# Kernel optimization log

Measured on AMD Instinct MI355X. Metric: run time of the kernel, lower is better.

Reference implementation:

```python
import jax, jax.numpy as jnp
import numpy as np

N_P, N_A, N_S, D = 50000, 25000, 1, 64
ALPHA = 0.2  # leaky_relu negative slope
E_P2P, E_P2A, E_A2P, E_A2A = 800000, 400000, 400000, 400000


def _gat(z_msg, wh_dst, aw, src, dst, n_dst):
    """Per-edge-type GAT: score = leaky_relu(attn_fc([z_src ; Wh_dst])),
    segment softmax over destination, weighted scatter-sum of z_src.
    Attention linear is split into src/dst halves and applied per-node (cheaper)."""
    d = z_msg.shape[1]
    e = (z_msg @ aw[:d])[src] + (wh_dst @ aw[d:])[dst]  # [E]
    e = jnp.where(e > 0, e, ALPHA * e)                   # leaky_relu
    m = jax.ops.segment_max(e, dst, num_segments=n_dst)
    ex = jnp.exp(e - m[dst])
    den = jax.ops.segment_sum(ex, dst, num_segments=n_dst)
    w = ex / den[dst]                                    # per-dst softmax (mailbox softmax)
    return jax.ops.segment_sum(w[:, None] * z_msg[src], dst, num_segments=n_dst)


def setup_inputs() -> dict:
    ks = jax.random.split(jax.random.key(0), 32)
    sc = 1.0 / np.sqrt(D)
    f32, i32 = jnp.float32, jnp.int32
    inp = {
        "feat_P": jax.random.normal(ks[0], (N_P, D), f32),
        "feat_A": jax.random.normal(ks[1], (N_A, D), f32),
        "feat_state": jax.random.normal(ks[2], (N_S, D), f32),
    }
    for i, n in enumerate(["P", "A", "p2p", "p2a", "a2p", "a2a", "p2s", "a2s", "in"]):
        inp["W_" + n] = jax.random.normal(ks[3 + i], (D, D), f32) * sc
        inp["b_" + n] = jnp.zeros((D,), f32)
    for i, n in enumerate(["p2p", "p2a", "a2p", "a2a", "p2s", "a2s"]):
        inp["a_" + n] = jax.random.normal(ks[12 + i], (2 * D,), f32) * sc
    inp["src_p2p"] = jax.random.randint(ks[18], (E_P2P,), 0, N_P, i32)
    inp["dst_p2p"] = jax.random.randint(ks[19], (E_P2P,), 0, N_P, i32)
    inp["src_p2a"] = jax.random.randint(ks[20], (E_P2A,), 0, N_P, i32)
    inp["dst_p2a"] = jax.random.randint(ks[21], (E_P2A,), 0, N_A, i32)
    inp["src_a2p"] = jax.random.randint(ks[22], (E_A2P,), 0, N_A, i32)
    inp["dst_a2p"] = jax.random.randint(ks[23], (E_A2P,), 0, N_P, i32)
    inp["src_a2a"] = jax.random.randint(ks[24], (E_A2A,), 0, N_A, i32)
    inp["dst_a2a"] = jax.random.randint(ks[25], (E_A2A,), 0, N_A, i32)
    inp["src_p2s"] = jnp.arange(N_P, dtype=i32)
    inp["dst_p2s"] = jnp.zeros((N_P,), i32)
    inp["src_a2s"] = jnp.arange(N_A, dtype=i32)
    inp["dst_a2s"] = jnp.zeros((N_A,), i32)
    return inp


def reference(feat_P, feat_A, feat_state,
              W_P, b_P, W_A, b_A, W_p2p, b_p2p, W_p2a, b_p2a, W_a2p, b_a2p,
              W_a2a, b_a2a, W_p2s, b_p2s, W_a2s, b_a2s, W_in, b_in,
              a_p2p, a_p2a, a_a2p, a_a2a, a_p2s, a_a2s,
              src_p2p, dst_p2p, src_p2a, dst_p2a, src_a2p, dst_a2p,
              src_a2a, dst_a2a, src_p2s, dst_p2s, src_a2s, dst_a2s):
    Wh_P = feat_P @ W_P + b_P          # self transform per node type
    Wh_A = feat_A @ W_A + b_A
    Wh_in = feat_state @ W_in + b_in   # 'in' self-loop message to state
    h_P = jax.nn.relu(
        Wh_P
        + _gat(feat_P @ W_p2p + b_p2p, Wh_P, a_p2p, src_p2p, dst_p2p, N_P)
        + _gat(feat_A @ W_a2p + b_a2p, Wh_P, a_a2p, src_a2p, dst_a2p, N_P))
    h_A = jax.nn.relu(
        Wh_A
        + _gat(feat_P @ W_p2a + b_p2a, Wh_A, a_p2a, src_p2a, dst_p2a, N_A)
        + _gat(feat_A @ W_a2a + b_a2a, Wh_A, a_a2a, src_a2a, dst_a2a, N_A))
    h_S = jax.nn.relu(
        Wh_in
        + _gat(feat_P @ W_p2s + b_p2s, Wh_in, a_p2s, src_p2s, dst_p2s, N_S)
        + _gat(feat_A @ W_a2s + b_a2s, Wh_in, a_a2s, src_a2s, dst_a2s, N_S))
    return (h_P, h_A, h_S)
```

## Files before the change

### kernel.cpp

```cpp
#include <hip/hip_runtime.h>
#include <math.h>

#define ALPHA 0.2f
#define NP 50000
#define NA 25000
#define NBINS 150000
#define ABASE 100000
#define NBUCK 586
#define CH 4096
#define CAP 8192
#define GP ((NP + 63) / 64)
#define GA ((NA + 63) / 64)
#define XS_LD 68

typedef unsigned short u16;
typedef __attribute__((ext_vector_type(8))) short bf16x8;
typedef __attribute__((ext_vector_type(8))) unsigned short u16x8;
typedef __attribute__((ext_vector_type(4))) float f32x4;

__device__ __forceinline__ float bf2f(u16 u) { return __uint_as_float(((unsigned)u) << 16); }
__device__ __forceinline__ u16 f2bf(float f) {
    unsigned x = __float_as_uint(f);
    return (u16)((x + 0x7fffu + ((x >> 16) & 1u)) >> 16);
}

struct FrontArgs {
    const float *feat_P, *feat_A, *feat_S;
    const float *W_P, *b_P, *W_A, *b_A, *W_p2p, *b_p2p, *W_p2a, *b_p2a,
                *W_a2p, *b_a2p, *W_a2a, *b_a2a, *W_p2s, *b_p2s, *W_a2s, *b_a2s,
                *W_in, *b_in;
    const float *a_p2p, *a_p2a, *a_a2p, *a_a2a, *a_p2s, *a_a2s;
    float *WhP, *WhA;
    u16 *z_p2p, *z_p2a, *z_a2p, *z_a2a;
    float *ss_p2p, *sd_p2p, *ss_p2a, *sd_p2a, *ss_a2p, *sd_a2p, *ss_a2a, *sd_a2a;
    float *outS, *den2, *numP, *numA;
    const int *src_p2p, *dst_p2p, *src_a2p, *dst_a2p,
              *src_p2a, *dst_p2a, *src_a2a, *dst_a2a;
    int E_p2p, E_a2p, E_p2a, E_a2a, E_tot, nblk;
    int *cursor0, *ebuf;
};

__device__ __forceinline__ void xform_body(int bid, float* __restrict__ Xs,
    const float* __restrict__ X, int N,
    const float* __restrict__ W0, const float* __restrict__ b0, float* __restrict__ Wh,
    const float* __restrict__ dA, float* __restrict__ sdA,
    const float* __restrict__ dB, float* __restrict__ sdB,
    const float* __restrict__ W1, const float* __restrict__ b1, u16* __restrict__ z1,
    const float* __restrict__ v1, float* __restrict__ s1,
    const float* __restrict__ W2, const float* __restrict__ b2, u16* __restrict__ z2,
    const float* __restrict__ v2, float* __restrict__ s2,
    const float* __restrict__ W3, const float* __restrict__ b3,
    const float* __restrict__ v3,
    const float* __restrict__ aD,
    const float* __restrict__ fS, const float* __restrict__ W_in, const float* __restrict__ b_in,
    float* __restrict__ num, float* __restrict__ den)
{
    int tid = threadIdx.x, wv = tid >> 6, lane = tid & 63;
    int g = lane >> 4, li = lane & 15;
    const float* Wm = wv == 0 ? W0 : wv == 1 ? W1 : wv == 2 ? W2 : W3;
    const float* bm = wv == 0 ? b0 : wv == 1 ? b1 : wv == 2 ? b2 : b3;
    const float* dv = wv == 0 ? dA : wv == 1 ? v1 : wv == 2 ? v2 : v3;
    float* sm       = wv == 0 ? sdA : wv == 1 ? s1 : wv == 2 ? s2 : nullptr;
    u16* zm         = wv == 1 ? z1 : wv == 2 ? z2 : nullptr;

    int base0 = bid * 64;
    for (int i = tid; i < 4096; i += 256) {
        int r = i >> 6, c = i & 63;
        int rowC = min(base0 + r, N - 1);
        Xs[r * XS_LD + c] = X[(long long)rowC * 64 + c];
    }

    bf16x8 Bf[4][2];
#pragma unroll
    for (int cb = 0; cb < 4; ++cb)
#pragma unroll
        for (int kc = 0; kc < 2; ++kc) {
            bf16x8 t;
#pragma unroll
            for (int j = 0; j < 8; ++j)
                t[j] = (short)f2bf(Wm[(kc * 32 + g * 8 + j) * 64 + cb * 16 + li]);
            Bf[cb][kc] = t;
        }
    float bl[4], dvl[4], dbl[4];
#pragma unroll
    for (int cb = 0; cb < 4; ++cb) {
        bl[cb]  = bm[cb * 16 + li];
        dvl[cb] = dv[cb * 16 + li];
        dbl[cb] = (wv == 0) ? dB[cb * 16 + li] : 0.f;
    }
    float sdst = 0.f;
    if (wv == 3) {
#pragma unroll
        for (int cb = 0; cb < 4; ++cb) {
            int c = cb * 16 + li;
            float a = b_in[c];
            for (int k = 0; k < 64; ++k) a = fmaf(fS[k], W_in[k * 64 + c], a);
            sdst = fmaf(a, aD[c], sdst);
        }
#pragma unroll
        for (int o = 1; o < 16; o <<= 1) sdst += __shfl_xor(sdst, o, 64);
    }
    float pnum[4] = {0.f, 0.f, 0.f, 0.f};
    float pden = 0.f;
    __syncthreads();

#pragma unroll
    for (int rt = 0; rt < 4; ++rt) {
        int rbase = base0 + rt * 16;
        if (rbase >= N) break;
        bf16x8 Af[2];
#pragma unroll
        for (int kc = 0; kc < 2; ++kc) {
            const float* xp = &Xs[(rt * 16 + li) * XS_LD + kc * 32 + g * 8];
            bf16x8 t;
#pragma unroll
            for (int j = 0; j < 8; ++j)
                t[j] = (short)f2bf(xp[j]);
            Af[kc] = t;
        }
        f32x4 acc[4] = {{0,0,0,0},{0,0,0,0},{0,0,0,0},{0,0,0,0}};
#pragma unroll
        for (int kc = 0; kc < 2; ++kc)
#pragma unroll
            for (int cb = 0; cb < 4; ++cb)
                acc[cb] = __builtin_amdgcn_mfma_f32_16x16x32_bf16(Af[kc], Bf[cb][kc], acc[cb], 0, 0, 0);
        float pd[4] = {0,0,0,0}, pb[4] = {0,0,0,0};
#pragma unroll
        for (int cb = 0; cb < 4; ++cb)
#pragma unroll
            for (int r = 0; r < 4; ++r) {
                float val = acc[cb][r] + bl[cb];
                acc[cb][r] = val;
                pd[r] = fmaf(val, dvl[cb], pd[r]);
                pb[r] = fmaf(val, dbl[cb], pb[r]);
            }
#pragma unroll
        for (int o = 1; o < 16; o <<= 1)
#pragma unroll
            for (int r = 0; r < 4; ++r) {
                pd[r] += __shfl_xor(pd[r], o, 64);
                pb[r] += __shfl_xor(pb[r], o, 64);
            }
        int rg = rbase + g * 4;
        if (wv == 3) {
#pragma unroll
            for (int r = 0; r < 4; ++r) {
                int row = rg + r;
                float e = pd[r] + sdst;
                e = e > 0.f ? e : ALPHA * e;
                float w = (row < N) ? __expf(e) : 0.f;
                pden += w;
#pragma unroll
                for (int cb = 0; cb < 4; ++cb)
                    pnum[cb] = fmaf(w, acc[cb][r], pnum[cb]);
            }
            continue;
        }
        if (li == 0) {
#pragma unroll
            for (int r = 0; r < 4; ++r) {
                int row = rg + r;
                if (row < N) {
                    sm[row] = pd[r];
                    if (wv == 0) sdB[row] = pb[r];
                }
            }
        }
        if (wv == 0) {
#pragma unroll
            for (int r = 0; r < 4; ++r) {
                int row = rg + r;
                if (row < N)
#pragma unroll
                    for (int cb = 0; cb < 4; ++cb)
                        Wh[(long long)row * 64 + cb * 16 + li] = acc[cb][r];
            }
        } else {
#pragma unroll
            for (int r = 0; r < 4; ++r) {
                int row = rg + r;
                if (row < N)
#pragma unroll
                    for (int cb = 0; cb < 4; ++cb)
                        zm[(long long)row * 64 + cb * 16 + li] = f2bf(acc[cb][r]);
            }
        }
    }
    if (wv == 3) {
#pragma unroll
        for (int o = 16; o <= 32; o <<= 1) {
            pden += __shfl_xor(pden, o, 64);
#pragma unroll
            for (int cb = 0; cb < 4; ++cb)
                pnum[cb] += __shfl_xor(pnum[cb], o, 64);
        }
        if (lane < 16) {
#pragma unroll
            for (int cb = 0; cb < 4; ++cb)
                atomicAdd(&num[cb * 16 + li], pnum[cb]);
            if (li == 0) atomicAdd(den, pden);
        }
    }
}

__device__ __forceinline__ void edge_decode(int k,
    const int* __restrict__ s0, const int* __restrict__ d0, int E0,
    const int* __restrict__ s1, const int* __restrict__ d1, int E1,
    const int* __restrict__ s2, const int* __restrict__ d2, int E2,
    const int* __restrict__ s3, const int* __restrict__ d3,
    int& src, int& bin) {
    if (k < E0) { src = s0[k]; bin = 2 * d0[k]; return; }
    k -= E0; if (k < E1) { src = s1[k]; bin = 2 * d1[k] + 1; return; }
    k -= E1; if (k < E2) { src = s2[k]; bin = ABASE + 2 * d2[k]; return; }
    k -= E2; src = s3[k]; bin = ABASE + 2 * d3[k] + 1;
}

__global__ __launch_bounds__(256) void fused_front(FrontArgs A) {
    __shared__ float smem[64 * XS_LD];
    int bid = blockIdx.x;
    int tid = threadIdx.x;
    if (bid < A.nblk) {
        int* h = (int*)smem;
        int* base = h + NBUCK;
        for (int i = tid; i < NBUCK; i += 256) h[i] = 0;
        __syncthreads();
        int b0 = bid * CH;
        int b1 = min(b0 + CH, A.E_tot);
        int cbin[16], csrc[16];
#pragma unroll
        for (int it = 0; it < 16; ++it) {
            int i = b0 + it * 256 + tid;
            int bin = -1, src = 0;
            if (i < b1)
                edge_decode(i, A.src_p2p, A.dst_p2p, A.E_p2p,
                            A.src_a2p, A.dst_a2p, A.E_a2p,
                            A.src_p2a, A.dst_p2a, A.E_p2a,
                            A.src_a2a, A.dst_a2a, src, bin);
            cbin[it] = bin; csrc[it] = src;
            if (bin >= 0) atomicAdd(&h[bin >> 8], 1);
        }
        __syncthreads();
        for (int i = tid; i < NBUCK; i += 256) {
            int c = h[i];
            base[i] = c ? (i * CAP + atomicAdd(&A.cursor0[i], c)) : 0;
            h[i] = 0;
        }
        __syncthreads();
#pragma unroll
        for (int it = 0; it < 16; ++it) {
            int bin = cbin[it];
            if (bin >= 0) {
                int bk = bin >> 8;
                int pos = base[bk] + atomicAdd(&h[bk], 1);
                if (pos < (bk + 1) * CAP)
                    A.ebuf[pos] = csrc[it] | ((bin & 255) << 16);
            }
        }
        return;
    }
    bid -= A.nblk;
    if (bid < GP) {
        xform_body(bid, smem, A.feat_P, NP,
                   A.W_P, A.b_P, A.WhP, A.a_p2p + 64, A.sd_p2p, A.a_a2p + 64, A.sd_a2p,
                   A.W_p2p, A.b_p2p, A.z_p2p, A.a_p2p, A.ss_p2p,
                   A.W_p2a, A.b_p2a, A.z_p2a, A.a_p2a, A.ss_p2a,
                   A.W_p2s, A.b_p2s, A.a_p2s, A.a_p2s + 64,
                   A.feat_S, A.W_in, A.b_in, A.numP, &A.den2[0]);
        return;
    }
    bid -= GP;
    if (bid < GA) {
        xform_body(bid, smem, A.feat_A, NA,
                   A.W_A, A.b_A, A.WhA, A.a_p2a + 64, A.sd_p2a, A.a_a2a + 64, A.sd_a2a,
                   A.W_a2p, A.b_a2p, A.z_a2p, A.a_a2p, A.ss_a2p,
                   A.W_a2a, A.b_a2a, A.z_a2a, A.a_a2a, A.ss_a2a,
                   A.W_a2s, A.b_a2s, A.a_a2s, A.a_a2s + 64,
                   A.feat_S, A.W_in, A.b_in, A.numA, &A.den2[1]);
        return;
    }
    if (tid < 64) {
        int c = tid;
        float acc = A.b_in[c];
        for (int k = 0; k < 64; ++k) acc = fmaf(A.feat_S[k], A.W_in[k * 64 + c], acc);
        A.outS[c] = acc;
    }
}

__device__ void scan_counts(const int* __restrict__ counts, int* sstart) {
    __shared__ int wtot_sb[4];
    int tid = threadIdx.x, lane = tid & 63, wv = tid >> 6;
    int carry = 0;
    for (int c = 0; c < 3; ++c) {
        int i = c * 256 + tid;
        int v = (i < NBUCK) ? min(counts[i], CAP) : 0;
        int x = v;
#pragma unroll
        for (int o = 1; o < 64; o <<= 1) {
            int y = __shfl_up(x, o, 64);
            if (lane >= o) x += y;
        }
        if (lane == 63) wtot_sb[wv] = x;
        __syncthreads();
        int woff = carry;
        for (int j = 0; j < wv; ++j) woff += wtot_sb[j];
        int ctot = wtot_sb[0] + wtot_sb[1] + wtot_sb[2] + wtot_sb[3];
        if (i < NBUCK) sstart[i] = x + woff - v;
        __syncthreads();
        carry += ctot;
    }
    if (tid == 0) sstart[NBUCK] = carry;
    __syncthreads();
}

__global__ __launch_bounds__(256) void fused_mid(
    const int* __restrict__ ebuf, const int* __restrict__ cursor0,
    int* __restrict__ ssrc, int* __restrict__ offs,
    const float* __restrict__ numP, const float* __restrict__ numA,
    const float* __restrict__ den2, float* __restrict__ outS) {
    int tid = threadIdx.x, lane = tid & 63, wv = tid >> 6;
    if ((int)blockIdx.x >= NBUCK) {
        if (tid < 64)
            outS[tid] = fmaxf(outS[tid] + numP[tid] / den2[0] + numA[tid] / den2[1], 0.f);
        return;
    }
    __shared__ int sstart[NBUCK + 1];
    __shared__ int lsrc[CAP];
    __shared__ int lcnt[256];
    __shared__ int loff[256];
    __shared__ int lcur[256];
    __shared__ int wtot[4];
    int b = blockIdx.x;
    scan_counts(cursor0, sstart);
    int pstart = sstart[b];
    int rstart = b * CAP;
    int cnt = min(cursor0[b], CAP);
    lcnt[tid] = 0;
    __syncthreads();
    for (int e = tid; e < cnt; e += 256)
        atomicAdd(&lcnt[((unsigned)ebuf[rstart + e]) >> 16], 1);
    __syncthreads();
    int v = lcnt[tid];
    int x = v;
#pragma unroll
    for (int o = 1; o < 64; o <<= 1) {
        int y = __shfl_up(x, o, 64);
        if (lane >= o) x += y;
    }
    if (lane == 63) wtot[wv] = x;
    __syncthreads();
    int woff = 0;
    for (int j = 0; j < wv; ++j) woff += wtot[j];
    int excl = x + woff - v;
    loff[tid] = excl;
    lcur[tid] = excl;
    __syncthreads();
    for (int e = tid; e < cnt; e += 256) {
        int val = ebuf[rstart + e];
        int pos = atomicAdd(&lcur[((unsigned)val) >> 16], 1);
        lsrc[pos] = val & 0xFFFF;
    }
    __syncthreads();
    for (int i = tid; i < cnt; i += 256) ssrc[pstart + i] = lsrc[i];
    int gb = b * 256 + tid;
    if (gb < NBINS) offs[gb] = pstart + loff[tid];
    if (b == 0 && tid == 0) offs[NBINS] = sstart[NBUCK];
}

__device__ __forceinline__ void seg_gat_g8(const int* __restrict__ ssrc, int s0, int s1,
                                           const float* __restrict__ ss, float sd,
                                           const u16* __restrict__ z, int lane,
                                           float* __restrict__ acc) {
    int cnt = s1 - s0;
    if (cnt <= 0) return;
    int egrp = lane >> 3, cg8 = (lane & 7) * 8;
    if (cnt <= 64) {
        int s = 0; float w = 0.f;
        if (lane < cnt) {
            s = ssrc[s0 + lane];
            float e = ss[s] + sd;
            e = e > 0.f ? e : ALPHA * e;
            w = __expf(e);
        }
        float den = w;
#pragma unroll
        for (int o = 32; o > 0; o >>= 1) den += __shfl_xor(den, o, 64);
        w *= 1.f / den;
        int nit = (cnt + 7) >> 3;
        for (int it = 0; it < nit; ++it) {
            int ei = it * 8 + egrp;
            float wt = __shfl(w, ei, 64);
            int   st = __shfl(s, ei, 64);
            u16x8 q = *(const u16x8*)(z + (long long)st * 64 + cg8);
#pragma unroll
            for (int j = 0; j < 8; ++j)
                acc[j] = fmaf(wt, bf2f(q[j]), acc[j]);
        }
    } else {
        float den = 0.f;
        for (int i = s0 + lane; i < s1; i += 64) {
            float e = ss[ssrc[i]] + sd; e = e > 0.f ? e : ALPHA * e; den += __expf(e);
        }
#pragma unroll
        for (int o = 32; o > 0; o >>= 1) den += __shfl_xor(den, o, 64);
        float inv = 1.f / den;
        for (int c = s0; c < s1; c += 64) {
            int i = c + lane; int s = 0; float w = 0.f;
            if (i < s1) {
                s = ssrc[i];
                float e = ss[s] + sd; e = e > 0.f ? e : ALPHA * e;
                w = __expf(e) * inv;
            }
            int cc = min(64, s1 - c);
            int nit = (cc + 7) >> 3;
            for (int it = 0; it < nit; ++it) {
                int ei = it * 8 + egrp;
                float wt = __shfl(w, ei, 64);
                int   st = __shfl(s, ei, 64);
                u16x8 q = *(const u16x8*)(z + (long long)st * 64 + cg8);
#pragma unroll
                for (int j = 0; j < 8; ++j)
                    acc[j] = fmaf(wt, bf2f(q[j]), acc[j]);
            }
        }
    }
}

__global__ __launch_bounds__(256) void gat_all(
    const int* __restrict__ ssrc, const int* __restrict__ offs,
    const float* __restrict__ WhP, float* __restrict__ outP,
    const float* __restrict__ WhA, float* __restrict__ outA,
    const float* __restrict__ ss_p2p, const float* __restrict__ sd_p2p, const u16* __restrict__ z_p2p,
    const float* __restrict__ ss_a2p, const float* __restrict__ sd_a2p, const u16* __restrict__ z_a2p,
    const float* __restrict__ ss_p2a, const float* __restrict__ sd_p2a, const u16* __restrict__ z_p2a,
    const float* __restrict__ ss_a2a, const float* __restrict__ sd_a2a, const u16* __restrict__ z_a2a) {
    int lane = threadIdx.x & 63;
    int g = (blockIdx.x * blockDim.x + threadIdx.x) >> 6;
    if (g >= NP + NA) return;
    bool isP = g < NP;
    int d = isP ? g : g - NP;
    int bin0 = isP ? 2 * d : ABASE + 2 * d;
    int e0 = offs[bin0], e1 = offs[bin0 + 1], e2 = offs[bin0 + 2];
    float acc[8] = {0.f, 0.f, 0.f, 0.f, 0.f, 0.f, 0.f, 0.f};
    if (isP) {
        seg_gat_g8(ssrc, e0, e1, ss_p2p, sd_p2p[d], z_p2p, lane, acc);
        seg_gat_g8(ssrc, e1, e2, ss_a2p, sd_a2p[d], z_a2p, lane, acc);
    } else {
        seg_gat_g8(ssrc, e0, e1, ss_p2a, sd_p2a[d], z_p2a, lane, acc);
        seg_gat_g8(ssrc, e1, e2, ss_a2a, sd_a2a[d], z_a2a, lane, acc);
    }
#pragma unroll
    for (int o = 8; o <= 32; o <<= 1)
#pragma unroll
        for (int j = 0; j < 8; ++j)
            acc[j] += __shfl_xor(acc[j], o, 64);
    if (lane < 8) {
        const float* Wh = isP ? WhP : WhA;
        float* outp = isP ? outP : outA;
        const float* sp = &Wh[(long long)d * 64 + lane * 8];
        float4 s0v = *(const float4*)sp;
        float4 s1v = *(const float4*)(sp + 4);
        float4 r0, r1;
        r0.x = fmaxf(s0v.x + acc[0], 0.f); r0.y = fmaxf(s0v.y + acc[1], 0.f);
        r0.z = fmaxf(s0v.z + acc[2], 0.f); r0.w = fmaxf(s0v.w + acc[3], 0.f);
        r1.x = fmaxf(s1v.x + acc[4], 0.f); r1.y = fmaxf(s1v.y + acc[5], 0.f);
        r1.z = fmaxf(s1v.z + acc[6], 0.f); r1.w = fmaxf(s1v.w + acc[7], 0.f);
        float* op = &outp[(long long)d * 64 + lane * 8];
        *(float4*)op = r0;
        *(float4*)(op + 4) = r1;
    }
}

extern "C" void kernel_launch(void* const* d_in, const int* in_sizes, int n_in,
                              void* d_out, int out_size, void* d_ws, size_t ws_size,
                              hipStream_t stream) {
    const float* feat_P = (const float*)d_in[0];
    const float* feat_A = (const float*)d_in[1];
    const float* feat_S = (const float*)d_in[2];
    const float* W_P   = (const float*)d_in[3];  const float* b_P   = (const float*)d_in[4];
    const float* W_A   = (const float*)d_in[5];  const float* b_A   = (const float*)d_in[6];
    const float* W_p2p = (const float*)d_in[7];  const float* b_p2p = (const float*)d_in[8];
    const float* W_p2a = (const float*)d_in[9];  const float* b_p2a = (const float*)d_in[10];
    const float* W_a2p = (const float*)d_in[11]; const float* b_a2p = (const float*)d_in[12];
    const float* W_a2a = (const float*)d_in[13]; const float* b_a2a = (const float*)d_in[14];
    const float* W_p2s = (const float*)d_in[15]; const float* b_p2s = (const float*)d_in[16];
    const float* W_a2s = (const float*)d_in[17]; const float* b_a2s = (const float*)d_in[18];
    const float* W_in  = (const float*)d_in[19]; const float* b_in  = (const float*)d_in[20];
    const float* a_p2p = (const float*)d_in[21];
    const float* a_p2a = (const float*)d_in[22];
    const float* a_a2p = (const float*)d_in[23];
    const float* a_a2a = (const float*)d_in[24];
    const float* a_p2s = (const float*)d_in[25];
    const float* a_a2s = (const float*)d_in[26];
    const int* src_p2p = (const int*)d_in[27]; const int* dst_p2p = (const int*)d_in[28];
    const int* src_p2a = (const int*)d_in[29]; const int* dst_p2a = (const int*)d_in[30];
    const int* src_a2p = (const int*)d_in[31]; const int* dst_a2p = (const int*)d_in[32];
    const int* src_a2a = (const int*)d_in[33]; const int* dst_a2a = (const int*)d_in[34];
    int E_p2p = in_sizes[27], E_p2a = in_sizes[29], E_a2p = in_sizes[31], E_a2a = in_sizes[33];
    int E_tot = E_p2p + E_a2p + E_p2a + E_a2a;

    float* out = (float*)d_out;
    float* outP = out;
    float* outA = out + (long long)NP * 64;
    float* outS = out + (long long)(NP + NA) * 64;

    float* ws = (float*)d_ws;
    float* WhP = ws; ws += (long long)NP * 64;
    float* WhA = ws; ws += (long long)NA * 64;
    u16* z_p2p = (u16*)ws; ws += (long long)NP * 32;
    u16* z_p2a = (u16*)ws; ws += (long long)NP * 32;
    u16* z_a2p = (u16*)ws; ws += (long long)NA * 32;
    u16* z_a2a = (u16*)ws; ws += (long long)NA * 32;
    float* ss_p2p = ws; ws += NP;  float* sd_p2p = ws; ws += NP;
    float* ss_p2a = ws; ws += NP;  float* sd_p2a = ws; ws += NA;
    float* ss_a2p = ws; ws += NA;  float* sd_a2p = ws; ws += NP;
    float* ss_a2a = ws; ws += NA;  float* sd_a2a = ws; ws += NA;
    float* zreg = ws;
    int*   cursor0 = (int*)ws; ws += NBUCK;
    float* den2 = ws; ws += 2;
    float* numP = ws; ws += 64;
    float* numA = ws; ws += 64;
    size_t zbytes = (size_t)((char*)ws - (char*)zreg);
    int* iw = (int*)ws;
    int* ebuf = iw; iw += NBUCK * CAP;
    int* ssrc = iw; iw += E_tot;
    int* offs = iw; iw += NBINS + 1;

    const int T = 256;
    int nblk = (E_tot + CH - 1) / CH;

    hipMemsetAsync(zreg, 0, zbytes, stream);

    FrontArgs FA;
    FA.feat_P = feat_P; FA.feat_A = feat_A; FA.feat_S = feat_S;
    FA.W_P = W_P; FA.b_P = b_P; FA.W_A = W_A; FA.b_A = b_A;
    FA.W_p2p = W_p2p; FA.b_p2p = b_p2p; FA.W_p2a = W_p2a; FA.b_p2a = b_p2a;
    FA.W_a2p = W_a2p; FA.b_a2p = b_a2p; FA.W_a2a = W_a2a; FA.b_a2a = b_a2a;
    FA.W_p2s = W_p2s; FA.b_p2s = b_p2s; FA.W_a2s = W_a2s; FA.b_a2s = b_a2s;
    FA.W_in = W_in; FA.b_in = b_in;
    FA.a_p2p = a_p2p; FA.a_p2a = a_p2a; FA.a_a2p = a_a2p; FA.a_a2a = a_a2a;
    FA.a_p2s = a_p2s; FA.a_a2s = a_a2s;
    FA.WhP = WhP; FA.WhA = WhA;
    FA.z_p2p = z_p2p; FA.z_p2a = z_p2a;
    FA.z_a2p = z_a2p; FA.z_a2a = z_a2a;
    FA.ss_p2p = ss_p2p; FA.sd_p2p = sd_p2p; FA.ss_p2a = ss_p2a; FA.sd_p2a = sd_p2a;
    FA.ss_a2p = ss_a2p; FA.sd_a2p = sd_a2p; FA.ss_a2a = ss_a2a; FA.sd_a2a = sd_a2a;
    FA.outS = outS; FA.den2 = den2; FA.numP = numP; FA.numA = numA;
    FA.src_p2p = src_p2p; FA.dst_p2p = dst_p2p; FA.src_a2p = src_a2p; FA.dst_a2p = dst_a2p;
    FA.src_p2a = src_p2a; FA.dst_p2a = dst_p2a; FA.src_a2a = src_a2a; FA.dst_a2a = dst_a2a;
    FA.E_p2p = E_p2p; FA.E_a2p = E_a2p; FA.E_p2a = E_p2a; FA.E_a2a = E_a2a;
    FA.E_tot = E_tot; FA.nblk = nblk;
    FA.cursor0 = cursor0; FA.ebuf = ebuf;
    fused_front<<<nblk + GP + GA + 1, T, 0, stream>>>(FA);

    fused_mid<<<NBUCK + 1, T, 0, stream>>>(ebuf, cursor0, ssrc, offs,
                                           numP, numA, den2, outS);

    gat_all<<<((NP + NA) * 64 + T - 1) / T, T, 0, stream>>>(ssrc, offs,
        WhP, outP, WhA, outA,
        ss_p2p, sd_p2p, z_p2p, ss_a2p, sd_a2p, z_a2p,
        ss_p2a, sd_p2a, z_p2a, ss_a2a, sd_a2a, z_a2a);
}
```

Before: 159.7 us.

## Reassociate state-node GAT through raw features and rebalance front/mid kernels

```diff
diff --git a/kernel.cpp b/kernel.cpp
--- a/kernel.cpp
+++ b/kernel.cpp
@@ -11,7 +11,8 @@
 #define CAP 8192
 #define GP ((NP + 63) / 64)
 #define GA ((NA + 63) / 64)
-#define XS_LD 68
+#define SB_P 384
+#define SB_A 192
 
 typedef unsigned short u16;
 typedef __attribute__((ext_vector_type(8))) short bf16x8;
@@ -24,184 +25,29 @@
     return (u16)((x + 0x7fffu + ((x >> 16) & 1u)) >> 16);
 }
 
-struct FrontArgs {
+struct K1Args {
+    const int *s0, *d0, *s1, *d1, *s2, *d2, *s3, *d3;
+    int E0, E1, E2, E3, Etot, nblk;
+    int *cursor0, *ebuf;
+    const float *feat_P, *feat_A, *feat_S;
+    const float *W_p2s, *b_p2s, *a_p2s, *W_a2s, *b_a2s, *a_a2s, *W_in, *b_in;
+    float *numP, *numA, *den2;
+};
+
+struct K2Args {
+    const int *ebuf; const int *cursor0;
+    int *ssrc; int *offs;
     const float *feat_P, *feat_A, *feat_S;
     const float *W_P, *b_P, *W_A, *b_A, *W_p2p, *b_p2p, *W_p2a, *b_p2a,
                 *W_a2p, *b_a2p, *W_a2a, *b_a2a, *W_p2s, *b_p2s, *W_a2s, *b_a2s,
                 *W_in, *b_in;
-    const float *a_p2p, *a_p2a, *a_a2p, *a_a2a, *a_p2s, *a_a2s;
+    const float *a_p2p, *a_p2a, *a_a2p, *a_a2a;
     float *WhP, *WhA;
     u16 *z_p2p, *z_p2a, *z_a2p, *z_a2a;
     float *ss_p2p, *sd_p2p, *ss_p2a, *sd_p2a, *ss_a2p, *sd_a2p, *ss_a2a, *sd_a2a;
-    float *outS, *den2, *numP, *numA;
-    const int *src_p2p, *dst_p2p, *src_a2p, *dst_a2p,
-              *src_p2a, *dst_p2a, *src_a2a, *dst_a2a;
-    int E_p2p, E_a2p, E_p2a, E_a2a, E_tot, nblk;
-    int *cursor0, *ebuf;
+    const float *numP, *numA, *den2;
+    float *outS;
 };
-
-__device__ __forceinline__ void xform_body(int bid, float* __restrict__ Xs,
-    const float* __restrict__ X, int N,
-    const float* __restrict__ W0, const float* __restrict__ b0, float* __restrict__ Wh,
-    const float* __restrict__ dA, float* __restrict__ sdA,
-    const float* __restrict__ dB, float* __restrict__ sdB,
-    const float* __restrict__ W1, const float* __restrict__ b1, u16* __restrict__ z1,
-    const float* __restrict__ v1, float* __restrict__ s1,
-    const float* __restrict__ W2, const float* __restrict__ b2, u16* __restrict__ z2,
-    const float* __restrict__ v2, float* __restrict__ s2,
-    const float* __restrict__ W3, const float* __restrict__ b3,
-    const float* __restrict__ v3,
-    const float* __restrict__ aD,
-    const float* __restrict__ fS, const float* __restrict__ W_in, const float* __restrict__ b_in,
-    float* __restrict__ num, float* __restrict__ den)
-{
-    int tid = threadIdx.x, wv = tid >> 6, lane = tid & 63;
-    int g = lane >> 4, li = lane & 15;
-    const float* Wm = wv == 0 ? W0 : wv == 1 ? W1 : wv == 2 ? W2 : W3;
-    const float* bm = wv == 0 ? b0 : wv == 1 ? b1 : wv == 2 ? b2 : b3;
-    const float* dv = wv == 0 ? dA : wv == 1 ? v1 : wv == 2 ? v2 : v3;
-    float* sm       = wv == 0 ? sdA : wv == 1 ? s1 : wv == 2 ? s2 : nullptr;
-    u16* zm         = wv == 1 ? z1 : wv == 2 ? z2 : nullptr;
-
-    int base0 = bid * 64;
-    for (int i = tid; i < 4096; i += 256) {
-        int r = i >> 6, c = i & 63;
-        int rowC = min(base0 + r, N - 1);
-        Xs[r * XS_LD + c] = X[(long long)rowC * 64 + c];
-    }
-
-    bf16x8 Bf[4][2];
-#pragma unroll
-    for (int cb = 0; cb < 4; ++cb)
-#pragma unroll
-        for (int kc = 0; kc < 2; ++kc) {
-            bf16x8 t;
-#pragma unroll
-            for (int j = 0; j < 8; ++j)
-                t[j] = (short)f2bf(Wm[(kc * 32 + g * 8 + j) * 64 + cb * 16 + li]);
-            Bf[cb][kc] = t;
-        }
-    float bl[4], dvl[4], dbl[4];
-#pragma unroll
-    for (int cb = 0; cb < 4; ++cb) {
-        bl[cb]  = bm[cb * 16 + li];
-        dvl[cb] = dv[cb * 16 + li];
-        dbl[cb] = (wv == 0) ? dB[cb * 16 + li] : 0.f;
-    }
-    float sdst = 0.f;
-    if (wv == 3) {
-#pragma unroll
-        for (int cb = 0; cb < 4; ++cb) {
-            int c = cb * 16 + li;
-            float a = b_in[c];
-            for (int k = 0; k < 64; ++k) a = fmaf(fS[k], W_in[k * 64 + c], a);
-            sdst = fmaf(a, aD[c], sdst);
-        }
-#pragma unroll
-        for (int o = 1; o < 16; o <<= 1) sdst += __shfl_xor(sdst, o, 64);
-    }
-    float pnum[4] = {0.f, 0.f, 0.f, 0.f};
-    float pden = 0.f;
-    __syncthreads();
-
-#pragma unroll
-    for (int rt = 0; rt < 4; ++rt) {
-        int rbase = base0 + rt * 16;
-        if (rbase >= N) break;
-        bf16x8 Af[2];
-#pragma unroll
-        for (int kc = 0; kc < 2; ++kc) {
-            const float* xp = &Xs[(rt * 16 + li) * XS_LD + kc * 32 + g * 8];
-            bf16x8 t;
-#pragma unroll
-            for (int j = 0; j < 8; ++j)
-                t[j] = (short)f2bf(xp[j]);
-            Af[kc] = t;
-        }
-        f32x4 acc[4] = {{0,0,0,0},{0,0,0,0},{0,0,0,0},{0,0,0,0}};
-#pragma unroll
-        for (int kc = 0; kc < 2; ++kc)
-#pragma unroll
-            for (int cb = 0; cb < 4; ++cb)
-                acc[cb] = __builtin_amdgcn_mfma_f32_16x16x32_bf16(Af[kc], Bf[cb][kc], acc[cb], 0, 0, 0);
-        float pd[4] = {0,0,0,0}, pb[4] = {0,0,0,0};
-#pragma unroll
-        for (int cb = 0; cb < 4; ++cb)
-#pragma unroll
-            for (int r = 0; r < 4; ++r) {
-                float val = acc[cb][r] + bl[cb];
-                acc[cb][r] = val;
-                pd[r] = fmaf(val, dvl[cb], pd[r]);
-                pb[r] = fmaf(val, dbl[cb], pb[r]);
-            }
-#pragma unroll
-        for (int o = 1; o < 16; o <<= 1)
-#pragma unroll
-            for (int r = 0; r < 4; ++r) {
-                pd[r] += __shfl_xor(pd[r], o, 64);
-                pb[r] += __shfl_xor(pb[r], o, 64);
-            }
-        int rg = rbase + g * 4;
-        if (wv == 3) {
-#pragma unroll
-            for (int r = 0; r < 4; ++r) {
-                int row = rg + r;
-                float e = pd[r] + sdst;
-                e = e > 0.f ? e : ALPHA * e;
-                float w = (row < N) ? __expf(e) : 0.f;
-                pden += w;
-#pragma unroll
-                for (int cb = 0; cb < 4; ++cb)
-                    pnum[cb] = fmaf(w, acc[cb][r], pnum[cb]);
-            }
-            continue;
-        }
-        if (li == 0) {
-#pragma unroll
-            for (int r = 0; r < 4; ++r) {
-                int row = rg + r;
-                if (row < N) {
-                    sm[row] = pd[r];
-                    if (wv == 0) sdB[row] = pb[r];
-                }
-            }
-        }
-        if (wv == 0) {
-#pragma unroll
-            for (int r = 0; r < 4; ++r) {
-                int row = rg + r;
-                if (row < N)
-#pragma unroll
-                    for (int cb = 0; cb < 4; ++cb)
-                        Wh[(long long)row * 64 + cb * 16 + li] = acc[cb][r];
-            }
-        } else {
-#pragma unroll
-            for (int r = 0; r < 4; ++r) {
-                int row = rg + r;
-                if (row < N)
-#pragma unroll
-                    for (int cb = 0; cb < 4; ++cb)
-                        zm[(long long)row * 64 + cb * 16 + li] = f2bf(acc[cb][r]);
-            }
-        }
-    }
-    if (wv == 3) {
-#pragma unroll
-        for (int o = 16; o <= 32; o <<= 1) {
-            pden += __shfl_xor(pden, o, 64);
-#pragma unroll
-            for (int cb = 0; cb < 4; ++cb)
-                pnum[cb] += __shfl_xor(pnum[cb], o, 64);
-        }
-        if (lane < 16) {
-#pragma unroll
-            for (int cb = 0; cb < 4; ++cb)
-                atomicAdd(&num[cb * 16 + li], pnum[cb]);
-            if (li == 0) atomicAdd(den, pden);
-        }
-    }
-}
 
 __device__ __forceinline__ void edge_decode(int k,
     const int* __restrict__ s0, const int* __restrict__ d0, int E0,
@@ -215,27 +61,24 @@
     k -= E2; src = s3[k]; bin = ABASE + 2 * d3[k] + 1;
 }
 
-__global__ __launch_bounds__(256) void fused_front(FrontArgs A) {
-    __shared__ float smem[64 * XS_LD];
+__global__ __launch_bounds__(256) void k1_kernel(K1Args A) {
+    __shared__ int h[NBUCK];
+    __shared__ int base[NBUCK];
     int bid = blockIdx.x;
     int tid = threadIdx.x;
     if (bid < A.nblk) {
-        int* h = (int*)smem;
-        int* base = h + NBUCK;
         for (int i = tid; i < NBUCK; i += 256) h[i] = 0;
         __syncthreads();
         int b0 = bid * CH;
-        int b1 = min(b0 + CH, A.E_tot);
+        int b1 = min(b0 + CH, A.Etot);
         int cbin[16], csrc[16];
 #pragma unroll
         for (int it = 0; it < 16; ++it) {
             int i = b0 + it * 256 + tid;
             int bin = -1, src = 0;
             if (i < b1)
-                edge_decode(i, A.src_p2p, A.dst_p2p, A.E_p2p,
-                            A.src_a2p, A.dst_a2p, A.E_a2p,
-                            A.src_p2a, A.dst_p2a, A.E_p2a,
-                            A.src_a2a, A.dst_a2a, src, bin);
+                edge_decode(i, A.s0, A.d0, A.E0, A.s1, A.d1, A.E1,
+                            A.s2, A.d2, A.E2, A.s3, A.d3, src, bin);
             cbin[it] = bin; csrc[it] = src;
             if (bin >= 0) atomicAdd(&h[bin >> 8], 1);
         }
@@ -258,32 +101,52 @@
         }
         return;
     }
-    bid -= A.nblk;
-    if (bid < GP) {
-        xform_body(bid, smem, A.feat_P, NP,
-                   A.W_P, A.b_P, A.WhP, A.a_p2p + 64, A.sd_p2p, A.a_a2p + 64, A.sd_a2p,
-                   A.W_p2p, A.b_p2p, A.z_p2p, A.a_p2p, A.ss_p2p,
-                   A.W_p2a, A.b_p2a, A.z_p2a, A.a_p2a, A.ss_p2a,
-                   A.W_p2s, A.b_p2s, A.a_p2s, A.a_p2s + 64,
-                   A.feat_S, A.W_in, A.b_in, A.numP, &A.den2[0]);
-        return;
-    }
-    bid -= GP;
-    if (bid < GA) {
-        xform_body(bid, smem, A.feat_A, NA,
-                   A.W_A, A.b_A, A.WhA, A.a_p2a + 64, A.sd_p2a, A.a_a2a + 64, A.sd_a2a,
-                   A.W_a2p, A.b_a2p, A.z_a2p, A.a_a2p, A.ss_a2p,
-                   A.W_a2a, A.b_a2a, A.z_a2a, A.a_a2a, A.ss_a2a,
-                   A.W_a2s, A.b_a2s, A.a_a2s, A.a_a2s + 64,
-                   A.feat_S, A.W_in, A.b_in, A.numA, &A.den2[1]);
-        return;
-    }
+    float* red = (float*)h;
+    int sb = bid - A.nblk;
+    bool isP = sb < SB_P;
+    int bidl = isP ? sb : sb - SB_P;
+    int nb = isP ? SB_P : SB_A;
+    int N = isP ? NP : NA;
+    const float* X   = isP ? A.feat_P : A.feat_A;
+    const float* W   = isP ? A.W_p2s  : A.W_a2s;
+    const float* b   = isP ? A.b_p2s  : A.b_a2s;
+    const float* a   = isP ? A.a_p2s  : A.a_a2s;
+    float* num       = isP ? A.numP   : A.numA;
+    float* den       = isP ? &A.den2[0] : &A.den2[1];
+    int lane = tid & 63, wv = tid >> 6;
+    float v = 0.f;
+    for (int c = 0; c < 64; ++c) v = fmaf(W[lane * 64 + c], a[c], v);
+    float t0 = b[lane] * a[lane];
+    float whc = A.b_in[lane];
+    for (int k = 0; k < 64; ++k) whc = fmaf(A.feat_S[k], A.W_in[k * 64 + lane], whc);
+    float t1 = whc * a[64 + lane];
+#pragma unroll
+    for (int o = 1; o < 64; o <<= 1) {
+        t0 += __shfl_xor(t0, o, 64);
+        t1 += __shfl_xor(t1, o, 64);
+    }
+    float cbias = t0 + t1;
+    float accx = 0.f, accd = 0.f;
+    int gw = bidl * 4 + wv, waves = nb * 4;
+    for (int r = gw; r < N; r += waves) {
+        float x = X[(long long)r * 64 + lane];
+        float ss = x * v;
+#pragma unroll
+        for (int o = 1; o < 64; o <<= 1) ss += __shfl_xor(ss, o, 64);
+        float e = ss + cbias;
+        e = e > 0.f ? e : ALPHA * e;
+        float w = __expf(e);
+        accx = fmaf(w, x, accx);
+        accd += w;
+    }
+    red[wv * 64 + lane] = accx;
+    if (lane == 0) red[256 + wv] = accd;
+    __syncthreads();
     if (tid < 64) {
-        int c = tid;
-        float acc = A.b_in[c];
-        for (int k = 0; k < 64; ++k) acc = fmaf(A.feat_S[k], A.W_in[k * 64 + c], acc);
-        A.outS[c] = acc;
-    }
+        float t = red[tid] + red[64 + tid] + red[128 + tid] + red[192 + tid];
+        atomicAdd(&num[tid], t);
+    }
+    if (tid == 64) atomicAdd(den, red[256] + red[257] + red[258] + red[259]);
 }
 
 __device__ void scan_counts(const int* __restrict__ counts, int* sstart) {
@@ -312,58 +175,194 @@
     __syncthreads();
 }
 
-__global__ __launch_bounds__(256) void fused_mid(
-    const int* __restrict__ ebuf, const int* __restrict__ cursor0,
-    int* __restrict__ ssrc, int* __restrict__ offs,
-    const float* __restrict__ numP, const float* __restrict__ numA,
-    const float* __restrict__ den2, float* __restrict__ outS) {
+__device__ __forceinline__ void xform_body3(int bid,
+    const float* __restrict__ X, int N,
+    const float* __restrict__ W0, const float* __restrict__ b0, float* __restrict__ Wh,
+    const float* __restrict__ dA, float* __restrict__ sdA,
+    const float* __restrict__ dB, float* __restrict__ sdB,
+    const float* __restrict__ W1, const float* __restrict__ b1, u16* __restrict__ z1,
+    const float* __restrict__ v1, float* __restrict__ s1,
+    const float* __restrict__ W2, const float* __restrict__ b2, u16* __restrict__ z2,
+    const float* __restrict__ v2, float* __restrict__ s2)
+{
+    int tid = threadIdx.x, wv = tid >> 6, lane = tid & 63;
+    if (wv == 3) return;
+    int g = lane >> 4, li = lane & 15;
+    const float* Wm = wv == 0 ? W0 : wv == 1 ? W1 : W2;
+    const float* bm = wv == 0 ? b0 : wv == 1 ? b1 : b2;
+    const float* dv = wv == 0 ? dA : wv == 1 ? v1 : v2;
+    float* sm       = wv == 0 ? sdA : wv == 1 ? s1 : s2;
+    u16* zm         = wv == 1 ? z1 : wv == 2 ? z2 : nullptr;
+
+    bf16x8 Bf[4][2];
+#pragma unroll
+    for (int cb = 0; cb < 4; ++cb)
+#pragma unroll
+        for (int kc = 0; kc < 2; ++kc) {
+            bf16x8 t;
+#pragma unroll
+            for (int j = 0; j < 8; ++j)
+                t[j] = (short)f2bf(Wm[(kc * 32 + g * 8 + j) * 64 + cb * 16 + li]);
+            Bf[cb][kc] = t;
+        }
+    float bl[4], dvl[4], dbl[4];
+#pragma unroll
+    for (int cb = 0; cb < 4; ++cb) {
+        bl[cb]  = bm[cb * 16 + li];
+        dvl[cb] = dv[cb * 16 + li];
+        dbl[cb] = (wv == 0) ? dB[cb * 16 + li] : 0.f;
+    }
+    int base0 = bid * 64;
+#pragma unroll
+    for (int rt = 0; rt < 4; ++rt) {
+        int rbase = base0 + rt * 16;
+        if (rbase >= N) break;
+        int rowC = min(rbase + li, N - 1);
+        bf16x8 Af[2];
+#pragma unroll
+        for (int kc = 0; kc < 2; ++kc) {
+            const float* xp = X + (long long)rowC * 64 + kc * 32 + g * 8;
+            float4 x0 = *(const float4*)xp;
+            float4 x1 = *(const float4*)(xp + 4);
+            bf16x8 t;
+            t[0] = (short)f2bf(x0.x); t[1] = (short)f2bf(x0.y);
+            t[2] = (short)f2bf(x0.z); t[3] = (short)f2bf(x0.w);
+            t[4] = (short)f2bf(x1.x); t[5] = (short)f2bf(x1.y);
+            t[6] = (short)f2bf(x1.z); t[7] = (short)f2bf(x1.w);
+            Af[kc] = t;
+        }
+        f32x4 acc[4] = {{0,0,0,0},{0,0,0,0},{0,0,0,0},{0,0,0,0}};
+#pragma unroll
+        for (int kc = 0; kc < 2; ++kc)
+#pragma unroll
+            for (int cb = 0; cb < 4; ++cb)
+                acc[cb] = __builtin_amdgcn_mfma_f32_16x16x32_bf16(Af[kc], Bf[cb][kc], acc[cb], 0, 0, 0);
+        float pd[4] = {0,0,0,0}, pb[4] = {0,0,0,0};
+#pragma unroll
+        for (int cb = 0; cb < 4; ++cb)
+#pragma unroll
+            for (int r = 0; r < 4; ++r) {
+                float val = acc[cb][r] + bl[cb];
+                acc[cb][r] = val;
+                pd[r] = fmaf(val, dvl[cb], pd[r]);
+                pb[r] = fmaf(val, dbl[cb], pb[r]);
+            }
+#pragma unroll
+        for (int o = 1; o < 16; o <<= 1)
+#pragma unroll
+            for (int r = 0; r < 4; ++r) {
+                pd[r] += __shfl_xor(pd[r], o, 64);
+                pb[r] += __shfl_xor(pb[r], o, 64);
+            }
+        int rg = rbase + g * 4;
+        if (li == 0) {
+#pragma unroll
+            for (int r = 0; r < 4; ++r) {
+                int row = rg + r;
+                if (row < N) {
+                    sm[row] = pd[r];
+                    if (wv == 0) sdB[row] = pb[r];
+                }
+            }
+        }
+        if (wv == 0) {
+#pragma unroll
+            for (int r = 0; r < 4; ++r) {
+                int row = rg + r;
+                if (row < N)
+#pragma unroll
+                    for (int cb = 0; cb < 4; ++cb)
+                        Wh[(long long)row * 64 + cb * 16 + li] = acc[cb][r];
+            }
+        } else {
+#pragma unroll
+            for (int r = 0; r < 4; ++r) {
+                int row = rg + r;
+                if (row < N)
+#pragma unroll
+                    for (int cb = 0; cb < 4; ++cb)
+                        zm[(long long)row * 64 + cb * 16 + li] = f2bf(acc[cb][r]);
+            }
+        }
+    }
+}
+
+__global__ __launch_bounds__(256) void k2_kernel(K2Args A) {
+    __shared__ int smem_i[NBUCK + 1 + 768 + 4];
+    __shared__ u16 lsrc[CAP];
+    int bid = blockIdx.x;
     int tid = threadIdx.x, lane = tid & 63, wv = tid >> 6;
-    if ((int)blockIdx.x >= NBUCK) {
-        if (tid < 64)
-            outS[tid] = fmaxf(outS[tid] + numP[tid] / den2[0] + numA[tid] / den2[1], 0.f);
+    if (bid < NBUCK) {
+        int* sstart = smem_i;
+        int* lcnt = smem_i + NBUCK + 1;
+        int* loff = lcnt + 256;
+        int* lcur = loff + 256;
+        int* wtot = lcur + 256;
+        int b = bid;
+        scan_counts(A.cursor0, sstart);
+        int pstart = sstart[b];
+        int rstart = b * CAP;
+        int cnt = min(A.cursor0[b], CAP);
+        lcnt[tid] = 0;
+        __syncthreads();
+        for (int e = tid; e < cnt; e += 256)
+            atomicAdd(&lcnt[((unsigned)A.ebuf[rstart + e]) >> 16], 1);
+        __syncthreads();
+        int v = lcnt[tid];
+        int x = v;
+#pragma unroll
+        for (int o = 1; o < 64; o <<= 1) {
+            int y = __shfl_up(x, o, 64);
+            if (lane >= o) x += y;
+        }
+        if (lane == 63) wtot[wv] = x;
+        __syncthreads();
+        int woff = 0;
+        for (int j = 0; j < wv; ++j) woff += wtot[j];
+        int excl = x + woff - v;
+        loff[tid] = excl;
+        lcur[tid] = excl;
+        __syncthreads();
+        for (int e = tid; e < cnt; e += 256) {
+            int val = A.ebuf[rstart + e];
+            int pos = atomicAdd(&lcur[((unsigned)val) >> 16], 1);
+            lsrc[pos] = (u16)(val & 0xFFFF);
+        }
+        __syncthreads();
+        for (int i = tid; i < cnt; i += 256) A.ssrc[pstart + i] = (int)lsrc[i];
+        int gb = b * 256 + tid;
+        if (gb < NBINS) A.offs[gb] = pstart + loff[tid];
+        if (b == 0 && tid == 0) A.offs[NBINS] = sstart[NBUCK];
         return;
     }
-    __shared__ int sstart[NBUCK + 1];
-    __shared__ int lsrc[CAP];
-    __shared__ int lcnt[256];
-    __shared__ int loff[256];
-    __shared__ int lcur[256];
-    __shared__ int wtot[4];
-    int b = blockIdx.x;
-    scan_counts(cursor0, sstart);
-    int pstart = sstart[b];
-    int rstart = b * CAP;
-    int cnt = min(cursor0[b], CAP);
-    lcnt[tid] = 0;
-    __syncthreads();
-    for (int e = tid; e < cnt; e += 256)
-        atomicAdd(&lcnt[((unsigned)ebuf[rstart + e]) >> 16], 1);
-    __syncthreads();
-    int v = lcnt[tid];
-    int x = v;
-#pragma unroll
-    for (int o = 1; o < 64; o <<= 1) {
-        int y = __shfl_up(x, o, 64);
-        if (lane >= o) x += y;
-    }
-    if (lane == 63) wtot[wv] = x;
-    __syncthreads();
-    int woff = 0;
-    for (int j = 0; j < wv; ++j) woff += wtot[j];
-    int excl = x + woff - v;
-    loff[tid] = excl;
-    lcur[tid] = excl;
-    __syncthreads();
-    for (int e = tid; e < cnt; e += 256) {
-        int val = ebuf[rstart + e];
-        int pos = atomicAdd(&lcur[((unsigned)val) >> 16], 1);
-        lsrc[pos] = val & 0xFFFF;
-    }
-    __syncthreads();
-    for (int i = tid; i < cnt; i += 256) ssrc[pstart + i] = lsrc[i];
-    int gb = b * 256 + tid;
-    if (gb < NBINS) offs[gb] = pstart + loff[tid];
-    if (b == 0 && tid == 0) offs[NBINS] = sstart[NBUCK];
+    bid -= NBUCK;
+    if (bid < GP) {
+        xform_body3(bid, A.feat_P, NP,
+                    A.W_P, A.b_P, A.WhP, A.a_p2p + 64, A.sd_p2p, A.a_a2p + 64, A.sd_a2p,
+                    A.W_p2p, A.b_p2p, A.z_p2p, A.a_p2p, A.ss_p2p,
+                    A.W_p2a, A.b_p2a, A.z_p2a, A.a_p2a, A.ss_p2a);
+        return;
+    }
+    bid -= GP;
+    if (bid < GA) {
+        xform_body3(bid, A.feat_A, NA,
+                    A.W_A, A.b_A, A.WhA, A.a_p2a + 64, A.sd_p2a, A.a_a2a + 64, A.sd_a2a,
+                    A.W_a2p, A.b_a2p, A.z_a2p, A.a_a2p, A.ss_a2p,
+                    A.W_a2a, A.b_a2a, A.z_a2a, A.a_a2a, A.ss_a2a);
+        return;
+    }
+    if (tid < 64) {
+        int c = tid;
+        float whc = A.b_in[c];
+        for (int k = 0; k < 64; ++k) whc = fmaf(A.feat_S[k], A.W_in[k * 64 + c], whc);
+        float mp = 0.f, ma = 0.f;
+        for (int k = 0; k < 64; ++k) {
+            mp = fmaf(A.numP[k], A.W_p2s[k * 64 + c], mp);
+            ma = fmaf(A.numA[k], A.W_a2s[k * 64 + c], ma);
+        }
+        float r = whc + mp / A.den2[0] + A.b_p2s[c] + ma / A.den2[1] + A.b_a2s[c];
+        A.outS[c] = fmaxf(r, 0.f);
+    }
 }
 
 __device__ __forceinline__ void seg_gat_g8(const int* __restrict__ ssrc, int s0, int s1,
@@ -530,30 +529,34 @@
 
     hipMemsetAsync(zreg, 0, zbytes, stream);
 
-    FrontArgs FA;
-    FA.feat_P = feat_P; FA.feat_A = feat_A; FA.feat_S = feat_S;
-    FA.W_P = W_P; FA.b_P = b_P; FA.W_A = W_A; FA.b_A = b_A;
-    FA.W_p2p = W_p2p; FA.b_p2p = b_p2p; FA.W_p2a = W_p2a; FA.b_p2a = b_p2a;
-    FA.W_a2p = W_a2p; FA.b_a2p = b_a2p; FA.W_a2a = W_a2a; FA.b_a2a = b_a2a;
-    FA.W_p2s = W_p2s; FA.b_p2s = b_p2s; FA.W_a2s = W_a2s; FA.b_a2s = b_a2s;
-    FA.W_in = W_in; FA.b_in = b_in;
-    FA.a_p2p = a_p2p; FA.a_p2a = a_p2a; FA.a_a2p = a_a2p; FA.a_a2a = a_a2a;
-    FA.a_p2s = a_p2s; FA.a_a2s = a_a2s;
-    FA.WhP = WhP; FA.WhA = WhA;
-    FA.z_p2p = z_p2p; FA.z_p2a = z_p2a;
-    FA.z_a2p = z_a2p; FA.z_a2a = z_a2a;
-    FA.ss_p2p = ss_p2p; FA.sd_p2p = sd_p2p; FA.ss_p2a = ss_p2a; FA.sd_p2a = sd_p2a;
-    FA.ss_a2p = ss_a2p; FA.sd_a2p = sd_a2p; FA.ss_a2a = ss_a2a; FA.sd_a2a = sd_a2a;
-    FA.outS = outS; FA.den2 = den2; FA.numP = numP; FA.numA = numA;
-    FA.src_p2p = src_p2p; FA.dst_p2p = dst_p2p; FA.src_a2p = src_a2p; FA.dst_a2p = dst_a2p;
-    FA.src_p2a = src_p2a; FA.dst_p2a = dst_p2a; FA.src_a2a = src_a2a; FA.dst_a2a = dst_a2a;
-    FA.E_p2p = E_p2p; FA.E_a2p = E_a2p; FA.E_p2a = E_p2a; FA.E_a2a = E_a2a;
-    FA.E_tot = E_tot; FA.nblk = nblk;
-    FA.cursor0 = cursor0; FA.ebuf = ebuf;
-    fused_front<<<nblk + GP + GA + 1, T, 0, stream>>>(FA);
-
-    fused_mid<<<NBUCK + 1, T, 0, stream>>>(ebuf, cursor0, ssrc, offs,
-                                           numP, numA, den2, outS);
+    K1Args K1;
+    K1.s0 = src_p2p; K1.d0 = dst_p2p; K1.s1 = src_a2p; K1.d1 = dst_a2p;
+    K1.s2 = src_p2a; K1.d2 = dst_p2a; K1.s3 = src_a2a; K1.d3 = dst_a2a;
+    K1.E0 = E_p2p; K1.E1 = E_a2p; K1.E2 = E_p2a; K1.E3 = E_a2a;
+    K1.Etot = E_tot; K1.nblk = nblk;
+    K1.cursor0 = cursor0; K1.ebuf = ebuf;
+    K1.feat_P = feat_P; K1.feat_A = feat_A; K1.feat_S = feat_S;
+    K1.W_p2s = W_p2s; K1.b_p2s = b_p2s; K1.a_p2s = a_p2s;
+    K1.W_a2s = W_a2s; K1.b_a2s = b_a2s; K1.a_a2s = a_a2s;
+    K1.W_in = W_in; K1.b_in = b_in;
+    K1.numP = numP; K1.numA = numA; K1.den2 = den2;
+    k1_kernel<<<nblk + SB_P + SB_A, T, 0, stream>>>(K1);
+
+    K2Args K2;
+    K2.ebuf = ebuf; K2.cursor0 = cursor0; K2.ssrc = ssrc; K2.offs = offs;
+    K2.feat_P = feat_P; K2.feat_A = feat_A; K2.feat_S = feat_S;
+    K2.W_P = W_P; K2.b_P = b_P; K2.W_A = W_A; K2.b_A = b_A;
+    K2.W_p2p = W_p2p; K2.b_p2p = b_p2p; K2.W_p2a = W_p2a; K2.b_p2a = b_p2a;
+    K2.W_a2p = W_a2p; K2.b_a2p = b_a2p; K2.W_a2a = W_a2a; K2.b_a2a = b_a2a;
+    K2.W_p2s = W_p2s; K2.b_p2s = b_p2s; K2.W_a2s = W_a2s; K2.b_a2s = b_a2s;
+    K2.W_in = W_in; K2.b_in = b_in;
+    K2.a_p2p = a_p2p; K2.a_p2a = a_p2a; K2.a_a2p = a_a2p; K2.a_a2a = a_a2a;
+    K2.WhP = WhP; K2.WhA = WhA;
+    K2.z_p2p = z_p2p; K2.z_p2a = z_p2a; K2.z_a2p = z_a2p; K2.z_a2a = z_a2a;
+    K2.ss_p2p = ss_p2p; K2.sd_p2p = sd_p2p; K2.ss_p2a = ss_p2a; K2.sd_p2a = sd_p2a;
+    K2.ss_a2p = ss_a2p; K2.sd_a2p = sd_a2p; K2.ss_a2a = ss_a2a; K2.sd_a2a = sd_a2a;
+    K2.numP = numP; K2.numA = numA; K2.den2 = den2; K2.outS = outS;
+    k2_kernel<<<NBUCK + GP + GA + 1, T, 0, stream>>>(K2);
 
     gat_all<<<((NP + NA) * 64 + T - 1) / T, T, 0, stream>>>(ssrc, offs,
         WhP, outP, WhA, outA,
```

Measured after the change: 131.6 us. -17.6%, faster.
